# Performance work log

Hardware: AMD Instinct MI355X
Metric: run time of the kernel (lower is better)

Reference implementation:

```python
import jax, jax.numpy as jnp
import numpy as np

N, E, F_IN, H, D = 50000, 800000, 128, 4, 32
NEG_SLOPE = 0.2

def setup_inputs() -> dict:
    key = jax.random.key(0)
    ks = jax.random.split(key, 8)
    x = jax.random.normal(ks[0], (N, F_IN), dtype=jnp.float32)
    src = jax.random.randint(ks[1], (E,), 0, N, dtype=jnp.int32)
    dst = jax.random.randint(ks[2], (E,), 0, N, dtype=jnp.int32)
    s = 1.0 / np.sqrt(F_IN)
    W_src = jax.random.uniform(ks[3], (F_IN, H * D), jnp.float32, -s, s)
    b_src = jnp.zeros((H * D,), jnp.float32)
    W_dst = jax.random.uniform(ks[4], (F_IN, H * D), jnp.float32, -s, s)
    b_dst = jnp.zeros((H * D,), jnp.float32)
    attn = jax.random.normal(ks[5], (H, D), dtype=jnp.float32) / np.sqrt(D)
    return {"x": x, "src": src, "dst": dst, "W_src": W_src, "b_src": b_src,
            "W_dst": W_dst, "b_dst": b_dst, "attn": attn}

def reference(x, src, dst, W_src, b_src, W_dst, b_dst, attn):
    n = x.shape[0]
    # dense projections: [N, H, D]
    fs = (x @ W_src + b_src).reshape(n, H, D)
    fd = (x @ W_dst + b_dst).reshape(n, H, D)
    # GATv2 edge score: a^T leaky_relu(W_l x_u + W_r x_v)
    e = jax.nn.leaky_relu(fs[src] + fd[dst], NEG_SLOPE)  # [E, H, D]
    score = jnp.einsum('ehd,hd->eh', e, attn)            # [E, H]
    # segment softmax over incoming edges of each dst node
    smax = jax.ops.segment_max(score, dst, num_segments=n)
    smax = jnp.where(jnp.isfinite(smax), smax, 0.0)
    ex = jnp.exp(score - smax[dst])
    denom = jax.ops.segment_sum(ex, dst, num_segments=n)
    alpha = ex / denom[dst]                              # [E, H]
    # scatter-weighted aggregation of src features
    h = jax.ops.segment_sum(alpha[:, :, None] * fs[src], dst, num_segments=n)
    h = jax.nn.relu(h)                                   # activation=relu
    return h.reshape(n, H * D)
```

## Files before the change

kernel.cpp:

```cpp
#include <hip/hip_runtime.h>
#include <hip/hip_fp16.h>

#define NN 50000
#define NE 800000
#define FIN 128
#define NH 4
#define HD 32
#define FOUT 128
#define NEG 0.2f
#define NB_W    ((256 * FIN + 255) / 256)
#define N_GEMM  782
#define NBKT    98
#define CHUNK   4096
#define NCHUNK  ((NE + CHUNK - 1) / CHUNK)
#define GB_GRID 980
#define BCAP    12288

typedef __attribute__((ext_vector_type(8))) short bf16x8;
typedef __attribute__((ext_vector_type(4))) float f32x4;

__device__ __forceinline__ uint f2bf_u(float f) {
    uint u = __float_as_uint(f);
    u += 0x7FFF + ((u >> 16) & 1);
    return u >> 16;
}
__device__ __forceinline__ ushort f2bf(float f) { return (ushort)f2bf_u(f); }
__device__ __forceinline__ uint f2h_u(float f) {
    return (uint)__builtin_bit_cast(ushort, __float2half(f));
}

template<int CTRL>
__device__ __forceinline__ float dpp_add(float x) {
    int y = __builtin_amdgcn_update_dpp(0, __float_as_int(x), CTRL, 0xF, 0xF, false);
    return x + __int_as_float(y);
}
#define DPP_QUAD_XOR1 0xB1
#define DPP_QUAD_XOR2 0x4E

__device__ __forceinline__ __half2 u2h(uint u) { return __builtin_bit_cast(__half2, u); }
__device__ __forceinline__ uint h2u(__half2 h) { return __builtin_bit_cast(uint, h); }

__device__ __forceinline__ __half2 hmax2(__half2 a, __half2 b) {
    uint r, ua = h2u(a), ub = h2u(b);
    asm("v_pk_max_f16 %0, %1, %2" : "=v"(r) : "v"(ua), "v"(ub));
    return u2h(r);
}

__global__ __launch_bounds__(256) void hist_wt_k(
    const int* __restrict__ dst, int* __restrict__ chunk_hist,
    const float* __restrict__ Wsrc, const float* __restrict__ Wdst,
    ushort* __restrict__ Wt,
    const float* __restrict__ attn, __half* __restrict__ attn_h)
{
    __shared__ int hist[NBKT];
    const int b = blockIdx.x;
    const int tid = threadIdx.x;
    if (b < NCHUNK) {
        const int e0 = b * CHUNK;
        for (int t = tid; t < NBKT; t += 256) hist[t] = 0;
        __syncthreads();
        #pragma unroll
        for (int k = 0; k < 16; ++k) {
            const int e = e0 + k * 256 + tid;
            if (e < NE) atomicAdd(&hist[dst[e] >> 9], 1);
        }
        __syncthreads();
        for (int t = tid; t < NBKT; t += 256)
            chunk_hist[b * NBKT + t] = hist[t];
    } else {
        if (b == NCHUNK && tid < FOUT) attn_h[tid] = __float2half(attn[tid]);
        int t = (b - NCHUNK) * 256 + tid;
        if (t >= 256 * FIN) return;
        int n = t >> 7, k = t & 127;
        float v = (n < 128) ? Wsrc[k * 128 + n] : Wdst[k * 128 + (n - 128)];
        Wt[t] = f2bf(v);
    }
}

__global__ __launch_bounds__(256) void gemm_scatter_k(
    const float* __restrict__ x, const ushort* __restrict__ Wt,
    const float* __restrict__ bsrc, const float* __restrict__ bdst,
    __half* __restrict__ fsfd,
    const int* __restrict__ dst, const int* __restrict__ src,
    const int* __restrict__ chunk_hist, int* __restrict__ bkbase,
    uint* __restrict__ ebuf)
{
    __shared__ ushort As[64 * 128];
    __shared__ int cur[NBKT];
    __shared__ int ps[256];
    const int b = blockIdx.x;
    const int tid = threadIdx.x;

    if (b % 5 == 0) {
        const int chunk = b / 5;
        int total = 0, part = 0;
        if (tid < NBKT) {
            for (int c = 0; c < NCHUNK; ++c) {
                const int h = chunk_hist[c * NBKT + tid];
                total += h;
                part += (c < chunk) ? h : 0;
            }
        }
        ps[tid] = (tid < NBKT) ? total : 0;
        __syncthreads();
        for (int off = 1; off < 256; off <<= 1) {
            int add = (tid >= off) ? ps[tid - off] : 0;
            __syncthreads();
            ps[tid] += add;
            __syncthreads();
        }
        if (tid < NBKT) cur[tid] = (ps[tid] - total) + part;
        if (chunk == 0) {
            if (tid < NBKT) bkbase[tid] = ps[tid] - total;
            if (tid == 0) bkbase[NBKT] = NE;
        }
        __syncthreads();
        const int e0 = chunk * CHUNK;
        #pragma unroll
        for (int k = 0; k < 16; ++k) {
            const int e = e0 + k * 256 + tid;
            if (e < NE) {
                const int d = dst[e];
                const int p = atomicAdd(&cur[d >> 9], 1);
                ebuf[p] = ((uint)d << 16) | (uint)src[e];
            }
        }
        return;
    }

    const int g = b - b / 5 - 1;
    if (g >= N_GEMM) return;
    const int bm = g * 64;

    for (int q = tid; q < 64 * 16; q += 256) {
        int r = q >> 4, c16 = q & 15;
        int row = bm + r;
        uint4 o = make_uint4(0u, 0u, 0u, 0u);
        if (row < NN) {
            const float4 a = *(const float4*)&x[(size_t)row * FIN + c16 * 8];
            const float4 c = *(const float4*)&x[(size_t)row * FIN + c16 * 8 + 4];
            o.x = f2bf_u(a.x) | (f2bf_u(a.y) << 16);
            o.y = f2bf_u(a.z) | (f2bf_u(a.w) << 16);
            o.z = f2bf_u(c.x) | (f2bf_u(c.y) << 16);
            o.w = f2bf_u(c.z) | (f2bf_u(c.w) << 16);
        }
        int off = r * 256 + ((c16 * 16) ^ ((r & 7) << 4));
        *(uint4*)((char*)As + off) = o;
    }
    __syncthreads();

    const int wid = tid >> 6, lane = tid & 63;
    const int wr = (wid >> 1) * 32, wc = (wid & 1) * 32;
    const int lrow = lane & 15;
    const int lk = (lane >> 4) * 16;
    const int kel = (lane >> 4) * 8;

    #pragma unroll
    for (int ct = 0; ct < 4; ++ct) {
        f32x4 acc[2][2] = {};
        #pragma unroll
        for (int kk = 0; kk < 4; ++kk) {
            bf16x8 a[2], bb[2];
            #pragma unroll
            for (int m = 0; m < 2; ++m) {
                int r = wr + m * 16 + lrow;
                int off = r * 256 + ((kk * 64 + lk) ^ ((r & 7) << 4));
                a[m] = *(bf16x8*)((char*)As + off);
            }
            #pragma unroll
            for (int n = 0; n < 2; ++n) {
                bb[n] = *(const bf16x8*)&Wt[(ct * 64 + wc + n * 16 + lrow) * FIN + kk * 32 + kel];
            }
            #pragma unroll
            for (int m = 0; m < 2; ++m)
                #pragma unroll
                for (int n = 0; n < 2; ++n)
                    acc[m][n] = __builtin_amdgcn_mfma_f32_16x16x32_bf16(bb[n], a[m], acc[m][n], 0, 0, 0);
        }

        #pragma unroll
        for (int m = 0; m < 2; ++m) {
            const int grow = bm + wr + m * 16 + (lane & 15);
            if (grow >= NN) continue;
            #pragma unroll
            for (int n = 0; n < 2; ++n) {
                const int gcolb = ct * 64 + wc + n * 16 + (lane >> 4) * 4;
                const float4 b4 = (gcolb < 128) ? *(const float4*)&bsrc[gcolb]
                                                : *(const float4*)&bdst[gcolb - 128];
                uint lo = f2h_u(acc[m][n][0] + b4.x) | (f2h_u(acc[m][n][1] + b4.y) << 16);
                uint hi = f2h_u(acc[m][n][2] + b4.z) | (f2h_u(acc[m][n][3] + b4.w) << 16);
                *(uint2*)&fsfd[(size_t)grow * 256 + gcolb] = make_uint2(lo, hi);
            }
        }
    }
}

__global__ __launch_bounds__(256) void binB_k(
    const uint* __restrict__ ebuf, const int* __restrict__ bkbase,
    int* __restrict__ rowptr, ushort* __restrict__ nbr)
{
    __shared__ int cnt_s[512];
    __shared__ int ps[256];
    __shared__ ushort buf[BCAP];
    const int b = blockIdx.x;
    const int tid = threadIdx.x;
    const int node0 = b << 9;
    const int nodes = (node0 + 512 < NN) ? 512 : (NN - node0);
    const int segbase = bkbase[b];
    const int segend  = bkbase[b + 1];
    const int seglen  = segend - segbase;

    cnt_s[tid] = 0;
    cnt_s[tid + 256] = 0;
    __syncthreads();
    for (int i = segbase + tid; i < segend; i += 256)
        atomicAdd(&cnt_s[(int)(ebuf[i] >> 16) - node0], 1);
    __syncthreads();

    const int c0 = cnt_s[2 * tid], c1 = cnt_s[2 * tid + 1];
    const int pair = c0 + c1;
    ps[tid] = pair;
    __syncthreads();
    for (int off = 1; off < 256; off <<= 1) {
        int add = (tid >= off) ? ps[tid - off] : 0;
        __syncthreads();
        ps[tid] += add;
        __syncthreads();
    }
    const int ex = ps[tid] - pair;
    __syncthreads();
    cnt_s[2 * tid] = ex;
    cnt_s[2 * tid + 1] = ex + c0;
    if (2 * tid < nodes)     rowptr[node0 + 2 * tid]     = segbase + ex;
    if (2 * tid + 1 < nodes) rowptr[node0 + 2 * tid + 1] = segbase + ex + c0;
    if (b == NBKT - 1 && tid == 0) rowptr[NN] = segend;
    __syncthreads();

    if (seglen <= BCAP) {
        for (int i = segbase + tid; i < segend; i += 256) {
            const uint e = ebuf[i];
            const int d = (int)(e >> 16) - node0;
            const int p = atomicAdd(&cnt_s[d], 1);
            buf[p] = (ushort)(e & 0xffffu);
        }
        __syncthreads();
        for (int i = tid; i < seglen; i += 256)
            nbr[segbase + i] = buf[i];
    } else {
        for (int i = segbase + tid; i < segend; i += 256) {
            const uint e = ebuf[i];
            const int d = (int)(e >> 16) - node0;
            const int p = atomicAdd(&cnt_s[d], 1);
            nbr[segbase + p] = (ushort)(e & 0xffffu);
        }
    }
}

__global__ __launch_bounds__(256) void gat_node_k(
    const __half* __restrict__ fsfd, const __half* __restrict__ attn_h,
    const int* __restrict__ rowptr, const ushort* __restrict__ nbr,
    float* __restrict__ out)
{
    const int node = blockIdx.x * 4 + (threadIdx.x >> 6);
    const int lane = threadIdx.x & 63;
    const int ql = lane & 15;
    const int q  = lane >> 4;

    const uint4 ufd = *(const uint4*)&fsfd[(size_t)node * 256 + 128 + 8 * ql];
    const __half2 fd0 = u2h(ufd.x), fd1 = u2h(ufd.y), fd2 = u2h(ufd.z), fd3 = u2h(ufd.w);
    const uint4 uav = *(const uint4*)&attn_h[8 * ql];
    const __half2 av0 = u2h(uav.x), av1 = u2h(uav.y), av2 = u2h(uav.z), av3 = u2h(uav.w);
    const __half2 k02 = __float2half2_rn(NEG);

    const int beg = rowptr[node];
    const int end = rowptr[node + 1];

    float den = 0.f;
    __half2 acc0 = u2h(0), acc1 = u2h(0), acc2 = u2h(0), acc3 = u2h(0);

    for (int i = beg; i < end; i += 16) {
        #pragma unroll
        for (int j = 0; j < 4; ++j) {
            const int idx = i + 4 * j + q;
            const bool valid = idx < end;
            const int s = nbr[valid ? idx : end - 1];
            const uint4 u = *(const uint4*)&fsfd[(size_t)s * 256 + 8 * ql];
            const __half2 f0 = u2h(u.x), f1 = u2h(u.y), f2 = u2h(u.z), f3 = u2h(u.w);
            __half2 v0 = __hadd2(f0, fd0), v1 = __hadd2(f1, fd1);
            __half2 v2 = __hadd2(f2, fd2), v3 = __hadd2(f3, fd3);
            v0 = hmax2(v0, __hmul2(v0, k02));
            v1 = hmax2(v1, __hmul2(v1, k02));
            v2 = hmax2(v2, __hmul2(v2, k02));
            v3 = hmax2(v3, __hmul2(v3, k02));
            __half2 sch = __hmul2(v0, av0);
            sch = __hfma2(v1, av1, sch);
            sch = __hfma2(v2, av2, sch);
            sch = __hfma2(v3, av3, sch);
            float sc = __low2float(sch) + __high2float(sch);
            sc = dpp_add<DPP_QUAD_XOR1>(sc);
            sc = dpp_add<DPP_QUAD_XOR2>(sc);
            float ex = __expf(sc);
            ex = valid ? ex : 0.f;
            den += ex;
            const __half2 exh = __float2half2_rn(ex);
            acc0 = __hfma2(exh, f0, acc0);
            acc1 = __hfma2(exh, f1, acc1);
            acc2 = __hfma2(exh, f2, acc2);
            acc3 = __hfma2(exh, f3, acc3);
        }
    }

    den += __shfl_xor(den, 16, 64);
    den += __shfl_xor(den, 32, 64);
    uint ua0 = h2u(acc0), ua1 = h2u(acc1), ua2 = h2u(acc2), ua3 = h2u(acc3);
    ua0 = h2u(__hadd2(u2h(ua0), u2h((uint)__shfl_xor((int)ua0, 16, 64))));
    ua1 = h2u(__hadd2(u2h(ua1), u2h((uint)__shfl_xor((int)ua1, 16, 64))));
    ua2 = h2u(__hadd2(u2h(ua2), u2h((uint)__shfl_xor((int)ua2, 16, 64))));
    ua3 = h2u(__hadd2(u2h(ua3), u2h((uint)__shfl_xor((int)ua3, 16, 64))));
    ua0 = h2u(__hadd2(u2h(ua0), u2h((uint)__shfl_xor((int)ua0, 32, 64))));
    ua1 = h2u(__hadd2(u2h(ua1), u2h((uint)__shfl_xor((int)ua1, 32, 64))));
    ua2 = h2u(__hadd2(u2h(ua2), u2h((uint)__shfl_xor((int)ua2, 32, 64))));
    ua3 = h2u(__hadd2(u2h(ua3), u2h((uint)__shfl_xor((int)ua3, 32, 64))));

    if (q == 0) {
        const float inv = (den > 0.f) ? 1.f / den : 0.f;
        float4 o0, o1;
        o0.x = fmaxf(__low2float(u2h(ua0))  * inv, 0.f);
        o0.y = fmaxf(__high2float(u2h(ua0)) * inv, 0.f);
        o0.z = fmaxf(__low2float(u2h(ua1))  * inv, 0.f);
        o0.w = fmaxf(__high2float(u2h(ua1)) * inv, 0.f);
        o1.x = fmaxf(__low2float(u2h(ua2))  * inv, 0.f);
        o1.y = fmaxf(__high2float(u2h(ua2)) * inv, 0.f);
        o1.z = fmaxf(__low2float(u2h(ua3))  * inv, 0.f);
        o1.w = fmaxf(__high2float(u2h(ua3)) * inv, 0.f);
        *(float4*)&out[(size_t)node * FOUT + 8 * ql] = o0;
        *(float4*)&out[(size_t)node * FOUT + 8 * ql + 4] = o1;
    }
}

extern "C" void kernel_launch(void* const* d_in, const int* in_sizes, int n_in,
                              void* d_out, int out_size, void* d_ws, size_t ws_size,
                              hipStream_t stream)
{
    const float* x    = (const float*)d_in[0];
    const int*   src  = (const int*)d_in[1];
    const int*   dst  = (const int*)d_in[2];
    const float* Wsrc = (const float*)d_in[3];
    const float* bsrc = (const float*)d_in[4];
    const float* Wdst = (const float*)d_in[5];
    const float* bdst = (const float*)d_in[6];
    const float* attn = (const float*)d_in[7];
    float* out = (float*)d_out;

    ushort* Wt      = (ushort*)d_ws;
    __half* fsfd    = (__half*)(Wt + 256 * FIN);
    int* chunk_hist = (int*)(fsfd + (size_t)NN * 256);
    int* bkbase     = chunk_hist + NCHUNK * NBKT;
    int* rowptr     = bkbase + NBKT + 1;
    uint* ebuf      = (uint*)(rowptr + NN + 1);
    ushort* nbr     = (ushort*)(ebuf + NE);
    __half* attn_h  = (__half*)(nbr + NE);

    hist_wt_k<<<NCHUNK + NB_W, 256, 0, stream>>>(dst, chunk_hist, Wsrc, Wdst, Wt, attn, attn_h);
    gemm_scatter_k<<<GB_GRID, 256, 0, stream>>>(x, Wt, bsrc, bdst, fsfd,
                                                dst, src, chunk_hist, bkbase, ebuf);
    binB_k<<<NBKT, 256, 0, stream>>>(ebuf, bkbase, rowptr, nbr);
    gat_node_k<<<(NN + 3) / 4, 256, 0, stream>>>(fsfd, attn_h, rowptr, nbr, out);
}
```

Measured before the change: 92.45 us.

## Stage edge scatter locally in LDS and tile weights through shared memory

The edge-bucketing blocks now count edges per bucket in LDS, run a local prefix scan, place the packed (dst,src) words contiguously in an LDS staging buffer, and then write them to ebuf in order. This replaces random global scattered writes with mostly coalesced ones. The GEMM blocks now load each 64-column weight tile into swizzled LDS before the MFMA loop instead of reading bf16 fragments straight from global memory. The cost is extra LDS usage, more barriers, and a second scan in the scatter blocks, which may lower occupancy.

New measurement: 86.93 us. -6.0%, faster.

```diff
diff --git a/kernel.cpp b/kernel.cpp
--- a/kernel.cpp
+++ b/kernel.cpp
@@ -86,13 +86,18 @@
     uint* __restrict__ ebuf)
 {
     __shared__ ushort As[64 * 128];
-    __shared__ int cur[NBKT];
+    __shared__ ushort Bs[64 * 128];
     __shared__ int ps[256];
+    __shared__ int gbase[NBKT];
+    __shared__ int lcur[NBKT];
+    __shared__ int delta[NBKT];
     const int b = blockIdx.x;
     const int tid = threadIdx.x;
 
     if (b % 5 == 0) {
         const int chunk = b / 5;
+        uint* stage = (uint*)As;
+
         int total = 0, part = 0;
         if (tid < NBKT) {
             for (int c = 0; c < NCHUNK; ++c) {
@@ -109,21 +114,56 @@
             ps[tid] += add;
             __syncthreads();
         }
-        if (tid < NBKT) cur[tid] = (ps[tid] - total) + part;
+        if (tid < NBKT) gbase[tid] = (ps[tid] - total) + part;
         if (chunk == 0) {
             if (tid < NBKT) bkbase[tid] = ps[tid] - total;
             if (tid == 0) bkbase[NBKT] = NE;
         }
-        __syncthreads();
+        if (tid < NBKT) lcur[tid] = 0;
+        __syncthreads();
+
         const int e0 = chunk * CHUNK;
+        int d[16], s[16];
         #pragma unroll
         for (int k = 0; k < 16; ++k) {
             const int e = e0 + k * 256 + tid;
             if (e < NE) {
-                const int d = dst[e];
-                const int p = atomicAdd(&cur[d >> 9], 1);
-                ebuf[p] = ((uint)d << 16) | (uint)src[e];
+                d[k] = dst[e];
+                s[k] = src[e];
+                atomicAdd(&lcur[d[k] >> 9], 1);
+            } else d[k] = -1;
+        }
+        __syncthreads();
+
+        const int lv = (tid < NBKT) ? lcur[tid] : 0;
+        ps[tid] = lv;
+        __syncthreads();
+        for (int off = 1; off < 256; off <<= 1) {
+            int add = (tid >= off) ? ps[tid - off] : 0;
+            __syncthreads();
+            ps[tid] += add;
+            __syncthreads();
+        }
+        if (tid < NBKT) {
+            const int loff = ps[tid] - lv;
+            lcur[tid] = loff;
+            delta[tid] = gbase[tid] - loff;
+        }
+        __syncthreads();
+
+        #pragma unroll
+        for (int k = 0; k < 16; ++k) {
+            if (d[k] >= 0) {
+                const int p = atomicAdd(&lcur[d[k] >> 9], 1);
+                stage[p] = ((uint)d[k] << 16) | (uint)s[k];
             }
+        }
+        __syncthreads();
+
+        const int cnt = (NE - e0 < CHUNK) ? (NE - e0) : CHUNK;
+        for (int i = tid; i < cnt; i += 256) {
+            const uint e = stage[i];
+            ebuf[delta[e >> 25] + i] = e;
         }
         return;
     }
@@ -147,16 +187,23 @@
         int off = r * 256 + ((c16 * 16) ^ ((r & 7) << 4));
         *(uint4*)((char*)As + off) = o;
     }
-    __syncthreads();
 
     const int wid = tid >> 6, lane = tid & 63;
     const int wr = (wid >> 1) * 32, wc = (wid & 1) * 32;
     const int lrow = lane & 15;
     const int lk = (lane >> 4) * 16;
-    const int kel = (lane >> 4) * 8;
 
     #pragma unroll
     for (int ct = 0; ct < 4; ++ct) {
+        if (ct > 0) __syncthreads();
+        for (int q = tid; q < 64 * 16; q += 256) {
+            int r = q >> 4, c16 = q & 15;
+            uint4 v = *(const uint4*)&Wt[(ct * 64 + r) * FIN + c16 * 8];
+            int off = r * 256 + ((c16 * 16) ^ ((r & 7) << 4));
+            *(uint4*)((char*)Bs + off) = v;
+        }
+        __syncthreads();
+
         f32x4 acc[2][2] = {};
         #pragma unroll
         for (int kk = 0; kk < 4; ++kk) {
@@ -169,7 +216,9 @@
             }
             #pragma unroll
             for (int n = 0; n < 2; ++n) {
-                bb[n] = *(const bf16x8*)&Wt[(ct * 64 + wc + n * 16 + lrow) * FIN + kk * 32 + kel];
+                int r = wc + n * 16 + lrow;
+                int off = r * 256 + ((kk * 64 + lk) ^ ((r & 7) << 4));
+                bb[n] = *(bf16x8*)((char*)Bs + off);
             }
             #pragma unroll
             for (int m = 0; m < 2; ++m)
```
